# Kernel tuning notes

Hardware: AMD Instinct MI355X
Metric: run time of the kernel (lower is better)

Reference implementation:

```python
import jax, jax.numpy as jnp
import numpy as np

N = 100000      # nodes
E = 800000      # edges
IN1 = 128       # gcn input feature dim
IN2 = 64        # lstm input feature dim
H = 128         # hidden_channels
B = 32          # lstm batch
T = 200         # lstm seq len
OUT = 1         # out_channels
TARGET = jnp.array([0, 1000, 2000, 3000, 4000, 5000, 6000, 7000])  # numgcnE=8


def setup_inputs() -> dict:
    key = jax.random.key(0)
    ks = jax.random.split(key, 20)
    s = 0.05
    inp = {
        "data0": jax.random.normal(ks[0], (B, T, IN2), jnp.float32),
        "data1": jax.random.normal(ks[1], (N, IN1), jnp.float32),
        "edge_index": jax.random.randint(ks[2], (2, E), 0, N, dtype=jnp.int64),
        # GCNConv layers (weight stored [in, out])
        "W1": jax.random.normal(ks[3], (IN1, H), jnp.float32) * s,
        "b1": jnp.zeros((H,), jnp.float32),
        "W2": jax.random.normal(ks[4], (H, H), jnp.float32) * s,
        "b2": jnp.zeros((H,), jnp.float32),
        # LSTM1 (gate order i,f,g,o as in torch)
        "Wih1": jax.random.normal(ks[5], (4 * H, IN2), jnp.float32) * s,
        "Whh1": jax.random.normal(ks[6], (4 * H, H), jnp.float32) * s,
        "bih1": jnp.zeros((4 * H,), jnp.float32),
        "bhh1": jnp.zeros((4 * H,), jnp.float32),
        # LSTM2
        "Wih2": jax.random.normal(ks[7], (4 * H, H), jnp.float32) * s,
        "Whh2": jax.random.normal(ks[8], (4 * H, H), jnp.float32) * s,
        "bih2": jnp.zeros((4 * H,), jnp.float32),
        "bhh2": jnp.zeros((4 * H,), jnp.float32),
        # MLP head: (numgcnE+1)*H -> (numgcnE+1)*H/2 -> OUT
        "m1_w": jax.random.normal(ks[9], (9 * H, 9 * H // 2), jnp.float32) * s,
        "m1_b": jnp.zeros((9 * H // 2,), jnp.float32),
        "m2_w": jax.random.normal(ks[10], (9 * H // 2, OUT), jnp.float32) * s,
        "m2_b": jnp.zeros((OUT,), jnp.float32),
    }
    return inp


def gcn_conv(x, W, b, src, dst, n):
    # PyG GCNConv: self-loops + symmetric normalization, then scatter-add.
    xw = x @ W                                                     # [N, H]
    ones = jnp.ones(src.shape[0], xw.dtype)
    deg = jax.ops.segment_sum(ones, dst, num_segments=n) + 1.0     # +1 self-loop
    dinv = jax.lax.rsqrt(deg)                                      # [N]
    norm = dinv[src] * dinv[dst]                                   # [E]
    agg = jax.ops.segment_sum(xw[src] * norm[:, None], dst, num_segments=n)
    agg = agg + xw * (dinv * dinv)[:, None]                        # self-loop msgs
    return agg + b


def lstm_final(x_tbi, Wih, Whh, bih, bhh):
    # x_tbi: [T, Bsz, in]; returns final hidden state h_T [Bsz, H]
    Bsz = x_tbi.shape[1]
    Hh = Whh.shape[1]
    bias = bih + bhh

    def step(carry, xt):
        h, c = carry
        g = xt @ Wih.T + h @ Whh.T + bias                          # [Bsz, 4H]
        i, f, gg, o = jnp.split(g, 4, axis=-1)
        c = jax.nn.sigmoid(f) * c + jax.nn.sigmoid(i) * jnp.tanh(gg)
        h = jax.nn.sigmoid(o) * jnp.tanh(c)
        return (h, c), None

    init = (jnp.zeros((Bsz, Hh), x_tbi.dtype), jnp.zeros((Bsz, Hh), x_tbi.dtype))
    (h, c), _ = jax.lax.scan(step, init, x_tbi)
    return h


def reference(data0, data1, edge_index, W1, b1, W2, b2,
              Wih1, Whh1, bih1, bhh1, Wih2, Whh2, bih2, bhh2,
              m1_w, m1_b, m2_w, m2_b):
    src, dst = edge_index[0], edge_index[1]
    n = data1.shape[0]
    # two GCN layers with ReLU
    h = jax.nn.relu(gcn_conv(data1, W1, b1, src, dst, n))
    h = jax.nn.relu(gcn_conv(h, W2, b2, src, dst, n))
    g = h[TARGET].reshape(-1)                                      # [numgcnE*H]
    # lstm1 over [B, T, IN2] (batch_first) -> final h_n [B, H]
    h1 = lstm_final(jnp.swapaxes(data0, 0, 1), Wih1, Whh1, bih1, bhh1)
    # lstm2 consumes h_n[None] as [batch=1, seq=B, H] -> final h [1, H]
    h2 = lstm_final(h1[:, None, :], Wih2, Whh2, bih2, bhh2)[0]     # [H]
    d = jnp.concatenate([g, h2])                                   # [(numgcnE+1)*H]
    return (d @ m1_w + m1_b) @ m2_w + m2_b                         # [OUT]
```

## Files before the change

### kernel.cpp

```cpp
#include <hip/hip_runtime.h>
#include <hip/hip_bf16.h>
#include <cstring>

using bf16 = __hip_bfloat16;
typedef _Float16 h2v __attribute__((ext_vector_type(2)));
typedef _Float16 h8v __attribute__((ext_vector_type(8)));

#if __has_builtin(__builtin_amdgcn_fdot2)
__device__ __forceinline__ float FDOT2(h2v a, h2v b, float c) {
    return __builtin_amdgcn_fdot2(a, b, c, false);
}
#else
__device__ __forceinline__ float FDOT2(h2v a, h2v b, float c) {
    return c + (float)a.x * (float)b.x + (float)a.y * (float)b.y;
}
#endif

__device__ __forceinline__ float sigm_f(float x) {
    return __builtin_amdgcn_rcpf(1.f + __expf(-x));
}
__device__ __forceinline__ float tanh_f(float x) {
    return 1.f - 2.f * __builtin_amdgcn_rcpf(1.f + __expf(2.f * x));
}

__device__ __forceinline__ float xor32_get(float x) {
#if __has_builtin(__builtin_amdgcn_permlane32_swap)
    typedef unsigned uv2 __attribute__((ext_vector_type(2)));
    union { float f; unsigned u; } cv; cv.f = x;
    uv2 r = __builtin_amdgcn_permlane32_swap(cv.u, cv.u, false, false);
    union { unsigned u; float f; } rv; rv.u = r[1];
    return rv.f;
#else
    return __shfl_xor(x, 32);
#endif
}

constexpr int NH    = 128;
constexpr int G4    = 512;
constexpr int TSEQ  = 200;
constexpr int BBATCH= 32;
constexpr int NTGT  = 8;

constexpr int LCAP1 = 1024;
constexpr int S1CAP = LCAP1 + NTGT;
constexpr int LCAP2 = 8192;
constexpr int S2CAP = LCAP2 + S1CAP;

constexpr size_t algn(size_t x) { return (x + 255) & ~size_t(255); }
constexpr size_t OFF_GX1  = 0;
constexpr size_t OFF_GX2  = algn(OFF_GX1  + 6400ull * G4 * 4);
constexpr size_t OFF_DEG  = algn(OFF_GX2  + 32ull * G4 * 4);
constexpr size_t OFF_DINV = algn(OFF_DEG  + 100000ull * 4);
constexpr size_t OFF_SL1  = algn(OFF_DINV + 100000ull * 4);
constexpr size_t OFF_SL2  = algn(OFF_SL1  + 100000ull * 4);
constexpr size_t OFF_CNT  = algn(OFF_SL2  + 100000ull * 4);
constexpr size_t OFF_L1   = algn(OFF_CNT  + 64);
constexpr size_t OFF_S1   = algn(OFF_L1   + (size_t)LCAP1 * 8);
constexpr size_t OFF_L2   = algn(OFF_S1   + (size_t)S1CAP * 4);
constexpr size_t OFF_S2   = algn(OFF_L2   + (size_t)LCAP2 * 8);
constexpr size_t OFF_XW1  = algn(OFF_S2   + (size_t)S2CAP * 4);
constexpr size_t OFF_H1   = algn(OFF_XW1  + (size_t)S2CAP * NH * 4);
constexpr size_t OFF_XW2  = algn(OFF_H1   + (size_t)S1CAP * NH * 4);
constexpr size_t OFF_DVEC = algn(OFF_XW2  + (size_t)S1CAP * NH * 4);
constexpr size_t OFF_H1F  = algn(OFF_DVEC + 1152ull * 4);
constexpr size_t OFF_CACC = algn(OFF_H1F  + 32ull * NH * 4);
constexpr size_t WS_NEEDED = OFF_CACC + 576ull * 4;

__device__ __forceinline__ int edge_at(const int* ei, int E, int is64, int row, int e) {
    return is64 ? ei[(((size_t)row * E) + e) * 2] : ei[((size_t)row * E) + e];
}

__device__ __forceinline__ float dinv_of(const int* deg, int v) {
    return rsqrtf((float)deg[v] + 1.0f);
}

__global__ void k_init(const int* ei, int* deg, int* slot1, int* slot2, int* cnt,
                       float* h1, int n, unsigned int* out, unsigned int canary) {
    int i0 = blockIdx.x * 256 + threadIdx.x;
    int gstride = gridDim.x * 256;
    if (i0 < 14) cnt[i0] = 0;
    if (i0 == 15) cnt[15] = (ei[1] == 0 && ei[3] == 0 && ei[5] == 0 && ei[7] == 0) ? 1 : 0;
    if (i0 == 16) out[0] = canary;
    for (int i = i0; i < S1CAP * NH; i += gstride) h1[i] = 0.f;
    for (int i = i0; i < n; i += gstride) { deg[i] = 0; slot1[i] = -1; slot2[i] = -1; }
}

__global__ void k_deg_l1(const int* ei, int E, int* deg, int2* l1, int* cnt) {
    int is64 = cnt[15];
    for (int e = blockIdx.x * 256 + threadIdx.x; e < E; e += gridDim.x * 256) {
        int d = edge_at(ei, E, is64, 1, e);
        if ((unsigned)d < 100000u) atomicAdd(&deg[d], 1);
        if (d <= 7000 && d >= 0 && d % 1000 == 0) {
            int s = edge_at(ei, E, is64, 0, e);
            int idx = atomicAdd(&cnt[0], 1);
            if (idx < LCAP1) l1[idx] = make_int2(s, d);
        }
    }
}

__global__ void k_s1(const int2* l1, int* cnt, int* slot1, int* s1list,
                     int* slot2, int* s2list) {
    __shared__ int ns1;
    if (threadIdx.x == 0) ns1 = 0;
    __syncthreads();
    int m = min(cnt[0], LCAP1);
    for (int i = threadIdx.x; i < NTGT + m; i += blockDim.x) {
        int v = (i < NTGT) ? i * 1000 : l1[i - NTGT].x;
        if ((unsigned)v >= 100000u) continue;
        int old = atomicCAS(&slot1[v], -1, -2);
        if (old == -1) {
            int idx = atomicAdd(&ns1, 1);
            if (idx < S1CAP) { s1list[idx] = v; atomicExch(&slot1[v], idx); }
        }
    }
    __syncthreads();
    int n1 = min(ns1, S1CAP);
    if (threadIdx.x == 0) cnt[1] = n1;
    for (int i = threadIdx.x; i < n1; i += blockDim.x) {
        int v = s1list[i];
        int old = atomicCAS(&slot2[v], -1, -2);
        if (old == -1) {
            int idx = atomicAdd(&cnt[2], 1);
            if (idx < S2CAP) { s2list[idx] = v; atomicExch(&slot2[v], idx); }
        }
    }
}

__global__ void k_l2(const int* ei, int E, const int* slot1,
                     int2* l2, int* cnt, int* slot2, int* s2list) {
    int is64 = cnt[15];
    for (int e = blockIdx.x * 256 + threadIdx.x; e < E; e += gridDim.x * 256) {
        int d = edge_at(ei, E, is64, 1, e);
        if ((unsigned)d >= 100000u) continue;
        if (slot1[d] >= 0) {
            int s = edge_at(ei, E, is64, 0, e);
            if ((unsigned)s >= 100000u) continue;
            int idx = atomicAdd(&cnt[3], 1);
            if (idx < LCAP2) l2[idx] = make_int2(s, d);
            int old = atomicCAS(&slot2[s], -1, -2);
            if (old == -1) {
                int j = atomicAdd(&cnt[2], 1);
                if (j < S2CAP) { s2list[j] = s; atomicExch(&slot2[s], j); }
            }
        }
    }
}


__global__ void k_xw1(const float* x, const float* W, const int* s2list, const int* cnt, float* xw1) {
    int i = blockIdx.x;
    if (i >= min(cnt[2], S2CAP)) return;
    int node = s2list[i];
    __shared__ float xs[NH];
    int c = threadIdx.x;
    xs[c] = x[(size_t)node * NH + c];
    __syncthreads();
    float acc = 0.f;
    #pragma unroll 8
    for (int k = 0; k < NH; k++) acc += xs[k] * W[(size_t)k * NH + c];
    xw1[(size_t)i * NH + c] = acc;
}

__global__ void k_h1scat(const float* xw1, const int2* l2, const int* cnt,
                         const int* slot1, const int* slot2, const int* deg, float* h1) {
    int e = blockIdx.x;
    if (e >= min(cnt[3], LCAP2)) return;
    int2 sd = l2[e];
    int t1 = slot1[sd.y], s2 = slot2[sd.x];
    if (t1 < 0 || t1 >= S1CAP || s2 < 0 || s2 >= S2CAP) return;
    float w = dinv_of(deg, sd.x) * dinv_of(deg, sd.y);
    atomicAdd(&h1[t1 * NH + threadIdx.x],
              xw1[(size_t)s2 * NH + threadIdx.x] * w);
}

__global__ void k_xw2(const float* h1, const float* xw1, const float* W, const float* b1,
                      const int* cnt, const int* s1list, const int* slot2, const int* deg,
                      float* xw2) {
    int i = blockIdx.x;
    if (i >= min(cnt[1], S1CAP)) return;
    __shared__ float xs[NH];
    int c = threadIdx.x;
    int node = s1list[i];
    int s2i = slot2[node];
    if (s2i < 0 || s2i >= S2CAP) s2i = 0;
    float v = dinv_of(deg, node);
    xs[c] = fmaxf(h1[i * NH + c] + xw1[(size_t)s2i * NH + c] * (v * v) + b1[c], 0.f);
    __syncthreads();
    float acc = 0.f;
    #pragma unroll 8
    for (int k = 0; k < NH; k++) acc += xs[k] * W[(size_t)k * NH + c];
    xw2[(size_t)i * NH + c] = acc;
}

__global__ void k_gout(const float* xw2, const int2* l1, const int* cnt,
                       const int* slot1, const int* deg, const float* b2, float* dvec) {
    int t = blockIdx.x;
    int tgt = t * 1000;
    int c = threadIdx.x;
    float vt = dinv_of(deg, tgt);
    int st = slot1[tgt]; if (st < 0 || st >= S1CAP) st = 0;
    float acc = xw2[(size_t)st * NH + c] * vt * vt;
    int m = min(cnt[0], LCAP1);
    for (int e = 0; e < m; e++) {
        int2 sd = l1[e];
        if (sd.y == tgt) {
            int ss = slot1[sd.x];
            if (ss >= 0 && ss < S1CAP)
                acc += xw2[(size_t)ss * NH + c] * dinv_of(deg, sd.x) * vt;
        }
    }
    acc += b2[c];
    dvec[t * NH + c] = fmaxf(acc, 0.f);
}


__global__ __launch_bounds__(256) void k_gx1hw(const float* data0, const float* Wih,
                                               const float* bih, const float* bhh, float* gx,
                                               const float* m1w, const float* m1b,
                                               const float* m2w, const float* m2b, float* hw) {
    int tid = threadIdx.x;
    if (blockIdx.x >= 800) {
        int hb = blockIdx.x - 800;
        int wv = tid >> 6, ln = tid & 63;
        if (hb < 18) {
            #pragma unroll 4
            for (int rr = 0; rr < 16; rr++) {
                int row = hb * 64 + wv * 16 + rr;
                float s = 0.f;
                #pragma unroll
                for (int j = ln; j < 576; j += 64) s += m1w[(size_t)row * 576 + j] * m2w[j];
                #pragma unroll
                for (int off = 32; off > 0; off >>= 1) s += __shfl_down(s, off, 64);
                if (ln == 0) hw[row] = s;
            }
        } else if (wv == 0) {
            float s = 0.f;
            for (int j = ln; j < 576; j += 64) s += m1b[j] * m2w[j];
            #pragma unroll
            for (int off = 32; off > 0; off >>= 1) s += __shfl_down(s, off, 64);
            if (ln == 0) hw[1152] = s + m2b[0];
        }
        return;
    }
    constexpr int LDP = 68;
    __shared__ float As[64 * LDP];
    __shared__ float Bs[64 * LDP];
    int rb = blockIdx.x >> 3;
    int gb = blockIdx.x & 7;
    int r0 = rb * 64, g0 = gb * 64;
    for (int i = tid; i < 64 * 64; i += 256) {
        int rr = i >> 6, k = i & 63;
        int r = r0 + rr, b = r & 31, t = r >> 5;
        As[rr * LDP + k] = data0[((size_t)b * TSEQ + t) * 64 + k];
        Bs[rr * LDP + k] = Wih[(size_t)(g0 + rr) * 64 + k];
    }
    __syncthreads();
    int tr = (tid & 15) * 4;
    int tg = (tid >> 4) * 4;
    float acc[4][4] = {};
    #pragma unroll
    for (int k4 = 0; k4 < 16; k4++) {
        float4 a0 = *(const float4*)&As[(tr + 0) * LDP + k4 * 4];
        float4 a1 = *(const float4*)&As[(tr + 1) * LDP + k4 * 4];
        float4 a2 = *(const float4*)&As[(tr + 2) * LDP + k4 * 4];
        float4 a3 = *(const float4*)&As[(tr + 3) * LDP + k4 * 4];
        float4 b0 = *(const float4*)&Bs[(tg + 0) * LDP + k4 * 4];
        float4 b1 = *(const float4*)&Bs[(tg + 1) * LDP + k4 * 4];
        float4 b2 = *(const float4*)&Bs[(tg + 2) * LDP + k4 * 4];
        float4 b3 = *(const float4*)&Bs[(tg + 3) * LDP + k4 * 4];
        const float4 av[4] = {a0, a1, a2, a3};
        const float4 bv[4] = {b0, b1, b2, b3};
        #pragma unroll
        for (int i = 0; i < 4; i++)
            #pragma unroll
            for (int j = 0; j < 4; j++)
                acc[i][j] += av[i].x * bv[j].x + av[i].y * bv[j].y
                           + av[i].z * bv[j].z + av[i].w * bv[j].w;
    }
    float bias[4];
    #pragma unroll
    for (int j = 0; j < 4; j++) bias[j] = bih[g0 + tg + j] + bhh[g0 + tg + j];
    #pragma unroll
    for (int i = 0; i < 4; i++) {
        size_t row = (size_t)(r0 + tr + i) * G4 + g0 + tg;
        #pragma unroll
        for (int j = 0; j < 4; j++) gx[row + j] = acc[i][j] + bias[j];
    }
}

template<int T, int NB>
__global__ __launch_bounds__(256, 1) void k_lstm1g(const float* gx, const float* Whh,
                                                   const float* Wih2, const float* bih2,
                                                   const float* bhh2, float* gx2) {
    int b = blockIdx.x;
    int tid = threadIdx.x;
    int w = tid >> 6, l = tid & 63;
    int j = w * 32 + (l & 31);
    int role = l >> 5;
    int r0 = role ? (j + NH) : j;
    int r1 = role ? (j + 3 * NH) : (j + 2 * NH);
    __shared__ __align__(16) _Float16 hbuf[2][NH];
    __shared__ float hfin[NH];
    h2v w0[NH / 2], w1[NH / 2];
    #pragma unroll
    for (int k = 0; k < NH; k += 4) {
        float4 a = *(const float4*)&Whh[(size_t)r0 * NH + k];
        w0[k / 2]     = h2v{(_Float16)a.x, (_Float16)a.y};
        w0[k / 2 + 1] = h2v{(_Float16)a.z, (_Float16)a.w};
        float4 c4 = *(const float4*)&Whh[(size_t)r1 * NH + k];
        w1[k / 2]     = h2v{(_Float16)c4.x, (_Float16)c4.y};
        w1[k / 2 + 1] = h2v{(_Float16)c4.z, (_Float16)c4.w};
    }
    if (tid < NH) { hbuf[0][tid] = (_Float16)0.f; hbuf[1][tid] = (_Float16)0.f; }
    float c = 0.f, hout = 0.f;
    float nx0 = gx[((size_t)0 * NB + b) * G4 + r0];
    float nx1 = gx[((size_t)0 * NB + b) * G4 + r1];
    __syncthreads();
    for (int t = 0; t < T; t++) {
        const h8v* hv8 = (const h8v*)hbuf[t & 1];
        float a0 = nx0, a1 = nx1;
        int tn = (t + 1 < T) ? (t + 1) : t;
        nx0 = gx[((size_t)tn * NB + b) * G4 + r0];
        nx1 = gx[((size_t)tn * NB + b) * G4 + r1];
        float p0 = 0.f, q0 = 0.f, p1 = 0.f, q1 = 0.f;
        #pragma unroll
        for (int m = 0; m < NH / 8; m++) {
            h8v h8 = hv8[m];
            h2v ha = __builtin_shufflevector(h8, h8, 0, 1);
            h2v hb = __builtin_shufflevector(h8, h8, 2, 3);
            h2v hc = __builtin_shufflevector(h8, h8, 4, 5);
            h2v hd = __builtin_shufflevector(h8, h8, 6, 7);
            p0 = FDOT2(w0[4 * m],     ha, p0);
            q0 = FDOT2(w0[4 * m + 1], hb, q0);
            p0 = FDOT2(w0[4 * m + 2], hc, p0);
            q0 = FDOT2(w0[4 * m + 3], hd, q0);
            p1 = FDOT2(w1[4 * m],     ha, p1);
            q1 = FDOT2(w1[4 * m + 1], hb, q1);
            p1 = FDOT2(w1[4 * m + 2], hc, p1);
            q1 = FDOT2(w1[4 * m + 3], hd, q1);
        }
        float ga = a0 + p0 + q0;
        float gb = a1 + p1 + q1;
        float s  = sigm_f(ga);
        float tg = role ? sigm_f(gb) : tanh_f(gb);
        float u  = s * tg;
        float fv = xor32_get(s);
        float ov = xor32_get(tg);
        if (role == 0) {
            c = fv * c + u;
            hout = ov * tanh_f(c);
            hbuf[(t + 1) & 1][j] = (_Float16)hout;
        }
        __syncthreads();
    }
    if (role == 0) hfin[j] = hout;
    __syncthreads();
    int g0 = tid, g1 = tid + 256;
    float a0 = bih2[g0] + bhh2[g0];
    float a1 = bih2[g1] + bhh2[g1];
    #pragma unroll 4
    for (int k = 0; k < NH; k++) {
        float hk = hfin[k];
        a0 += Wih2[(size_t)g0 * NH + k] * hk;
        a1 += Wih2[(size_t)g1 * NH + k] * hk;
    }
    gx2[(size_t)b * G4 + g0] = a0;
    gx2[(size_t)b * G4 + g1] = a1;
}

__global__ __launch_bounds__(256, 1) void k_lstm2h(const float* gx, const float* Whh,
                                                   const float* dvec, const float* hw,
                                                   unsigned int* out) {
    constexpr int T = BBATCH;
    int tid = threadIdx.x;
    int w = tid >> 6, l = tid & 63;
    int j = w * 32 + (l & 31);
    int role = l >> 5;
    int r0 = role ? (j + NH) : j;
    int r1 = role ? (j + 3 * NH) : (j + 2 * NH);
    __shared__ __align__(16) _Float16 hbuf[2][NH];
    __shared__ float harr[NH];
    __shared__ float red[4];
    h2v w0[NH / 2], w1[NH / 2];
    #pragma unroll
    for (int k = 0; k < NH; k += 4) {
        float4 a = *(const float4*)&Whh[(size_t)r0 * NH + k];
        w0[k / 2]     = h2v{(_Float16)a.x, (_Float16)a.y};
        w0[k / 2 + 1] = h2v{(_Float16)a.z, (_Float16)a.w};
        float4 c4 = *(const float4*)&Whh[(size_t)r1 * NH + k];
        w1[k / 2]     = h2v{(_Float16)c4.x, (_Float16)c4.y};
        w1[k / 2 + 1] = h2v{(_Float16)c4.z, (_Float16)c4.w};
    }
    if (tid < NH) { hbuf[0][tid] = (_Float16)0.f; hbuf[1][tid] = (_Float16)0.f; }
    float c = 0.f, hout = 0.f;
    float nx0 = gx[r0];
    float nx1 = gx[r1];
    __syncthreads();
    for (int t = 0; t < T; t++) {
        const h8v* hv8 = (const h8v*)hbuf[t & 1];
        float a0 = nx0, a1 = nx1;
        int tn = (t + 1 < T) ? (t + 1) : t;
        nx0 = gx[(size_t)tn * G4 + r0];
        nx1 = gx[(size_t)tn * G4 + r1];
        float p0 = 0.f, q0 = 0.f, p1 = 0.f, q1 = 0.f;
        #pragma unroll
        for (int m = 0; m < NH / 8; m++) {
            h8v h8 = hv8[m];
            h2v ha = __builtin_shufflevector(h8, h8, 0, 1);
            h2v hb = __builtin_shufflevector(h8, h8, 2, 3);
            h2v hc = __builtin_shufflevector(h8, h8, 4, 5);
            h2v hd = __builtin_shufflevector(h8, h8, 6, 7);
            p0 = FDOT2(w0[4 * m],     ha, p0);
            q0 = FDOT2(w0[4 * m + 1], hb, q0);
            p0 = FDOT2(w0[4 * m + 2], hc, p0);
            q0 = FDOT2(w0[4 * m + 3], hd, q0);
            p1 = FDOT2(w1[4 * m],     ha, p1);
            q1 = FDOT2(w1[4 * m + 1], hb, q1);
            p1 = FDOT2(w1[4 * m + 2], hc, p1);
            q1 = FDOT2(w1[4 * m + 3], hd, q1);
        }
        float ga = a0 + p0 + q0;
        float gb = a1 + p1 + q1;
        float s  = sigm_f(ga);
        float tg = role ? sigm_f(gb) : tanh_f(gb);
        float u  = s * tg;
        float fv = xor32_get(s);
        float ov = xor32_get(tg);
        if (role == 0) {
            c = fv * c + u;
            hout = ov * tanh_f(c);
            hbuf[(t + 1) & 1][j] = (_Float16)hout;
        }
        __syncthreads();
    }
    if (role == 0) harr[j] = hout;
    __syncthreads();
    float s = 0.f;
    for (int i = tid; i < 1024; i += 256) s += dvec[i] * hw[i];
    if (tid < NH) s += harr[tid] * hw[1024 + tid];
    #pragma unroll
    for (int off = 32; off > 0; off >>= 1) s += __shfl_down(s, off, 64);
    if ((tid & 63) == 0) red[tid >> 6] = s;
    __syncthreads();
    if (tid == 0) {
        float tot = red[0] + red[1] + red[2] + red[3] + hw[1152];
        bf16 hb = __float2bfloat16(tot);
        unsigned short u;
        memcpy(&u, &hb, 2);
        out[0] = ((unsigned int)u << 16) | u;
    }
}


extern "C" void kernel_launch(void* const* d_in, const int* in_sizes, int n_in,
                              void* d_out, int out_size, void* d_ws, size_t ws_size,
                              hipStream_t stream) {
    const float* data0 = (const float*)d_in[0];
    const float* data1 = (const float*)d_in[1];
    const int*   ei    = (const int*)d_in[2];
    const float* W1    = (const float*)d_in[3];
    const float* b1    = (const float*)d_in[4];
    const float* W2    = (const float*)d_in[5];
    const float* b2    = (const float*)d_in[6];
    const float* Wih1  = (const float*)d_in[7];
    const float* Whh1  = (const float*)d_in[8];
    const float* bih1  = (const float*)d_in[9];
    const float* bhh1  = (const float*)d_in[10];
    const float* Wih2  = (const float*)d_in[11];
    const float* Whh2  = (const float*)d_in[12];
    const float* bih2  = (const float*)d_in[13];
    const float* bhh2  = (const float*)d_in[14];
    const float* m1w   = (const float*)d_in[15];
    const float* m1b   = (const float*)d_in[16];
    const float* m2w   = (const float*)d_in[17];
    const float* m2b   = (const float*)d_in[18];

    const int n = in_sizes[1] / NH;
    const int E = in_sizes[2] / 2;

    char* ws = (char*)d_ws;
    float* gx1   = (float*)(ws + OFF_GX1);
    float* gx2   = (float*)(ws + OFF_GX2);
    int*   deg   = (int*)  (ws + OFF_DEG);
    float* hw    = (float*)(ws + OFF_DINV);
    int*   slot1 = (int*)  (ws + OFF_SL1);
    int*   slot2 = (int*)  (ws + OFF_SL2);
    int*   cnt   = (int*)  (ws + OFF_CNT);
    int2*  l1    = (int2*) (ws + OFF_L1);
    int*   s1l   = (int*)  (ws + OFF_S1);
    int2*  l2    = (int2*) (ws + OFF_L2);
    int*   s2l   = (int*)  (ws + OFF_S2);
    float* xw1   = (float*)(ws + OFF_XW1);
    float* h1    = (float*)(ws + OFF_H1);
    float* xw2   = (float*)(ws + OFF_XW2);
    float* dvec  = (float*)(ws + OFF_DVEC);

    float v = 1.0f + (ws_size < WS_NEEDED ? 1.0f : 0.0f) + (n_in != 19 ? 2.0f : 0.0f);
    unsigned int fb; memcpy(&fb, &v, 4);
    unsigned int hi = fb >> 16;
    unsigned int canary_bits = (hi << 16) | hi;

    int nb = (n + 255) / 256;
    int eb = (E + 255) / 256;

    k_init   <<<nb, 256, 0, stream>>>(ei, deg, slot1, slot2, cnt, h1, n,
                                      (unsigned int*)d_out, canary_bits);
    k_deg_l1 <<<eb, 256, 0, stream>>>(ei, E, deg, l1, cnt);
    k_s1     <<<1, 256, 0, stream>>>(l1, cnt, slot1, s1l, slot2, s2l);
    k_l2     <<<eb, 256, 0, stream>>>(ei, E, slot1, l2, cnt, slot2, s2l);
    k_xw1    <<<S2CAP, NH, 0, stream>>>(data1, W1, s2l, cnt, xw1);
    k_h1scat <<<LCAP2, NH, 0, stream>>>(xw1, l2, cnt, slot1, slot2, deg, h1);
    k_xw2    <<<S1CAP, NH, 0, stream>>>(h1, xw1, W2, b1, cnt, s1l, slot2, deg, xw2);
    k_gout   <<<NTGT, NH, 0, stream>>>(xw2, l1, cnt, slot1, deg, b2, dvec);
    k_gx1hw  <<<819, 256, 0, stream>>>(data0, Wih1, bih1, bhh1, gx1,
                                       m1w, m1b, m2w, m2b, hw);
    k_lstm1g<TSEQ, BBATCH><<<BBATCH, 256, 0, stream>>>(gx1, Whh1, Wih2, bih2, bhh2, gx2);
    k_lstm2h <<<1, 256, 0, stream>>>(gx2, Whh2, dvec, hw, (unsigned int*)d_out);
    (void)out_size;
}
```

Before: 421.8 us.

## Split LSTM recurrence over K halves with permlane reduction instead of gate rows

Each lane pair now computes all four gates for a hidden unit over half of the K dimension, and the two halves are combined with permlane32_swap sums. Before, each lane handled two gate rows over the full K. This halves the LDS h-vector reads per lane per step and shortens the dot-product chains, at the cost of extra cross-lane swaps per step. The xor32_get helper is rewritten to derive the partner value from the swap results, and the Wih2 projection uses float4 loads.

After: 419.1 us. About the same (-0.6%).

```diff
diff --git a/kernel.cpp b/kernel.cpp
--- a/kernel.cpp
+++ b/kernel.cpp
@@ -28,10 +28,22 @@
     typedef unsigned uv2 __attribute__((ext_vector_type(2)));
     union { float f; unsigned u; } cv; cv.f = x;
     uv2 r = __builtin_amdgcn_permlane32_swap(cv.u, cv.u, false, false);
-    union { unsigned u; float f; } rv; rv.u = r[1];
-    return rv.f;
+    union { unsigned u; float f; } ra, rb; ra.u = r[0]; rb.u = r[1];
+    return (ra.f + rb.f) - x;
 #else
     return __shfl_xor(x, 32);
+#endif
+}
+
+__device__ __forceinline__ float half_sum(float x) {
+#if __has_builtin(__builtin_amdgcn_permlane32_swap)
+    typedef unsigned uv2 __attribute__((ext_vector_type(2)));
+    union { float f; unsigned u; } cv; cv.f = x;
+    uv2 r = __builtin_amdgcn_permlane32_swap(cv.u, cv.u, false, false);
+    union { unsigned u; float f; } ra, rb; ra.u = r[0]; rb.u = r[1];
+    return ra.f + rb.f;
+#else
+    return x + __shfl_xor(x, 32);
 #endif
 }
 
@@ -296,73 +308,95 @@
     int tid = threadIdx.x;
     int w = tid >> 6, l = tid & 63;
     int j = w * 32 + (l & 31);
-    int role = l >> 5;
-    int r0 = role ? (j + NH) : j;
-    int r1 = role ? (j + 3 * NH) : (j + 2 * NH);
+    int hf = l >> 5;
+    int k0 = hf * 64;
     __shared__ __align__(16) _Float16 hbuf[2][NH];
     __shared__ float hfin[NH];
-    h2v w0[NH / 2], w1[NH / 2];
+    h2v wi[32], wf[32], wg[32], wo[32];
     #pragma unroll
-    for (int k = 0; k < NH; k += 4) {
-        float4 a = *(const float4*)&Whh[(size_t)r0 * NH + k];
-        w0[k / 2]     = h2v{(_Float16)a.x, (_Float16)a.y};
-        w0[k / 2 + 1] = h2v{(_Float16)a.z, (_Float16)a.w};
-        float4 c4 = *(const float4*)&Whh[(size_t)r1 * NH + k];
-        w1[k / 2]     = h2v{(_Float16)c4.x, (_Float16)c4.y};
-        w1[k / 2 + 1] = h2v{(_Float16)c4.z, (_Float16)c4.w};
+    for (int k = 0; k < 64; k += 4) {
+        float4 a;
+        a = *(const float4*)&Whh[(size_t)j * NH + k0 + k];
+        wi[k / 2] = h2v{(_Float16)a.x, (_Float16)a.y};
+        wi[k / 2 + 1] = h2v{(_Float16)a.z, (_Float16)a.w};
+        a = *(const float4*)&Whh[(size_t)(j + NH) * NH + k0 + k];
+        wf[k / 2] = h2v{(_Float16)a.x, (_Float16)a.y};
+        wf[k / 2 + 1] = h2v{(_Float16)a.z, (_Float16)a.w};
+        a = *(const float4*)&Whh[(size_t)(j + 2 * NH) * NH + k0 + k];
+        wg[k / 2] = h2v{(_Float16)a.x, (_Float16)a.y};
+        wg[k / 2 + 1] = h2v{(_Float16)a.z, (_Float16)a.w};
+        a = *(const float4*)&Whh[(size_t)(j + 3 * NH) * NH + k0 + k];
+        wo[k / 2] = h2v{(_Float16)a.x, (_Float16)a.y};
+        wo[k / 2 + 1] = h2v{(_Float16)a.z, (_Float16)a.w};
     }
     if (tid < NH) { hbuf[0][tid] = (_Float16)0.f; hbuf[1][tid] = (_Float16)0.f; }
     float c = 0.f, hout = 0.f;
-    float nx0 = gx[((size_t)0 * NB + b) * G4 + r0];
-    float nx1 = gx[((size_t)0 * NB + b) * G4 + r1];
+    const float* gp0 = &gx[(size_t)b * G4];
+    float nx0 = gp0[j], nx1 = gp0[j + NH], nx2 = gp0[j + 2 * NH], nx3 = gp0[j + 3 * NH];
     __syncthreads();
     for (int t = 0; t < T; t++) {
-        const h8v* hv8 = (const h8v*)hbuf[t & 1];
-        float a0 = nx0, a1 = nx1;
+        const h8v* hv8 = (const h8v*)&hbuf[t & 1][k0];
+        float a0 = nx0, a1 = nx1, a2 = nx2, a3 = nx3;
         int tn = (t + 1 < T) ? (t + 1) : t;
-        nx0 = gx[((size_t)tn * NB + b) * G4 + r0];
-        nx1 = gx[((size_t)tn * NB + b) * G4 + r1];
-        float p0 = 0.f, q0 = 0.f, p1 = 0.f, q1 = 0.f;
+        const float* gp = &gx[((size_t)tn * NB + b) * G4];
+        nx0 = gp[j]; nx1 = gp[j + NH]; nx2 = gp[j + 2 * NH]; nx3 = gp[j + 3 * NH];
+        float pi = 0.f, qi = 0.f, pf = 0.f, qf = 0.f;
+        float pg = 0.f, qg = 0.f, po = 0.f, qo = 0.f;
         #pragma unroll
-        for (int m = 0; m < NH / 8; m++) {
+        for (int m = 0; m < 8; m++) {
             h8v h8 = hv8[m];
             h2v ha = __builtin_shufflevector(h8, h8, 0, 1);
             h2v hb = __builtin_shufflevector(h8, h8, 2, 3);
             h2v hc = __builtin_shufflevector(h8, h8, 4, 5);
             h2v hd = __builtin_shufflevector(h8, h8, 6, 7);
-            p0 = FDOT2(w0[4 * m],     ha, p0);
-            q0 = FDOT2(w0[4 * m + 1], hb, q0);
-            p0 = FDOT2(w0[4 * m + 2], hc, p0);
-            q0 = FDOT2(w0[4 * m + 3], hd, q0);
-            p1 = FDOT2(w1[4 * m],     ha, p1);
-            q1 = FDOT2(w1[4 * m + 1], hb, q1);
-            p1 = FDOT2(w1[4 * m + 2], hc, p1);
-            q1 = FDOT2(w1[4 * m + 3], hd, q1);
-        }
-        float ga = a0 + p0 + q0;
-        float gb = a1 + p1 + q1;
-        float s  = sigm_f(ga);
-        float tg = role ? sigm_f(gb) : tanh_f(gb);
+            pi = FDOT2(wi[4 * m],     ha, pi);
+            qi = FDOT2(wi[4 * m + 1], hb, qi);
+            pi = FDOT2(wi[4 * m + 2], hc, pi);
+            qi = FDOT2(wi[4 * m + 3], hd, qi);
+            pf = FDOT2(wf[4 * m],     ha, pf);
+            qf = FDOT2(wf[4 * m + 1], hb, qf);
+            pf = FDOT2(wf[4 * m + 2], hc, pf);
+            qf = FDOT2(wf[4 * m + 3], hd, qf);
+            pg = FDOT2(wg[4 * m],     ha, pg);
+            qg = FDOT2(wg[4 * m + 1], hb, qg);
+            pg = FDOT2(wg[4 * m + 2], hc, pg);
+            qg = FDOT2(wg[4 * m + 3], hd, qg);
+            po = FDOT2(wo[4 * m],     ha, po);
+            qo = FDOT2(wo[4 * m + 1], hb, qo);
+            po = FDOT2(wo[4 * m + 2], hc, po);
+            qo = FDOT2(wo[4 * m + 3], hd, qo);
+        }
+        float gi = a0 + half_sum(pi + qi);
+        float gf = a1 + half_sum(pf + qf);
+        float gg = a2 + half_sum(pg + qg);
+        float go = a3 + half_sum(po + qo);
+        float s  = sigm_f(hf ? gf : gi);
+        float tg = hf ? sigm_f(go) : tanh_f(gg);
         float u  = s * tg;
         float fv = xor32_get(s);
         float ov = xor32_get(tg);
-        if (role == 0) {
+        if (hf == 0) {
             c = fv * c + u;
             hout = ov * tanh_f(c);
             hbuf[(t + 1) & 1][j] = (_Float16)hout;
         }
         __syncthreads();
     }
-    if (role == 0) hfin[j] = hout;
+    if (hf == 0) hfin[j] = hout;
     __syncthreads();
     int g0 = tid, g1 = tid + 256;
     float a0 = bih2[g0] + bhh2[g0];
     float a1 = bih2[g1] + bhh2[g1];
-    #pragma unroll 4
-    for (int k = 0; k < NH; k++) {
-        float hk = hfin[k];
-        a0 += Wih2[(size_t)g0 * NH + k] * hk;
-        a1 += Wih2[(size_t)g1 * NH + k] * hk;
+    const float4* w0p = (const float4*)&Wih2[(size_t)g0 * NH];
+    const float4* w1p = (const float4*)&Wih2[(size_t)g1 * NH];
+    const float4* hp  = (const float4*)hfin;
+    #pragma unroll 8
+    for (int k4 = 0; k4 < NH / 4; k4++) {
+        float4 h4 = hp[k4];
+        float4 wa = w0p[k4];
+        float4 wb = w1p[k4];
+        a0 += wa.x * h4.x + wa.y * h4.y + wa.z * h4.z + wa.w * h4.w;
+        a1 += wb.x * h4.x + wb.y * h4.y + wb.z * h4.z + wb.w * h4.w;
     }
     gx2[(size_t)b * G4 + g0] = a0;
     gx2[(size_t)b * G4 + g1] = a1;
@@ -375,65 +409,81 @@
     int tid = threadIdx.x;
     int w = tid >> 6, l = tid & 63;
     int j = w * 32 + (l & 31);
-    int role = l >> 5;
-    int r0 = role ? (j + NH) : j;
-    int r1 = role ? (j + 3 * NH) : (j + 2 * NH);
+    int hf = l >> 5;
+    int k0 = hf * 64;
     __shared__ __align__(16) _Float16 hbuf[2][NH];
     __shared__ float harr[NH];
     __shared__ float red[4];
-    h2v w0[NH / 2], w1[NH / 2];
+    h2v wi[32], wf[32], wg[32], wo[32];
     #pragma unroll
-    for (int k = 0; k < NH; k += 4) {
-        float4 a = *(const float4*)&Whh[(size_t)r0 * NH + k];
-        w0[k / 2]     = h2v{(_Float16)a.x, (_Float16)a.y};
-        w0[k / 2 + 1] = h2v{(_Float16)a.z, (_Float16)a.w};
-        float4 c4 = *(const float4*)&Whh[(size_t)r1 * NH + k];
-        w1[k / 2]     = h2v{(_Float16)c4.x, (_Float16)c4.y};
-        w1[k / 2 + 1] = h2v{(_Float16)c4.z, (_Float16)c4.w};
+    for (int k = 0; k < 64; k += 4) {
+        float4 a;
+        a = *(const float4*)&Whh[(size_t)j * NH + k0 + k];
+        wi[k / 2] = h2v{(_Float16)a.x, (_Float16)a.y};
+        wi[k / 2 + 1] = h2v{(_Float16)a.z, (_Float16)a.w};
+        a = *(const float4*)&Whh[(size_t)(j + NH) * NH + k0 + k];
+        wf[k / 2] = h2v{(_Float16)a.x, (_Float16)a.y};
+        wf[k / 2 + 1] = h2v{(_Float16)a.z, (_Float16)a.w};
+        a = *(const float4*)&Whh[(size_t)(j + 2 * NH) * NH + k0 + k];
+        wg[k / 2] = h2v{(_Float16)a.x, (_Float16)a.y};
+        wg[k / 2 + 1] = h2v{(_Float16)a.z, (_Float16)a.w};
+        a = *(const float4*)&Whh[(size_t)(j + 3 * NH) * NH + k0 + k];
+        wo[k / 2] = h2v{(_Float16)a.x, (_Float16)a.y};
+        wo[k / 2 + 1] = h2v{(_Float16)a.z, (_Float16)a.w};
     }
     if (tid < NH) { hbuf[0][tid] = (_Float16)0.f; hbuf[1][tid] = (_Float16)0.f; }
     float c = 0.f, hout = 0.f;
-    float nx0 = gx[r0];
-    float nx1 = gx[r1];
+    float nx0 = gx[j], nx1 = gx[j + NH], nx2 = gx[j + 2 * NH], nx3 = gx[j + 3 * NH];
     __syncthreads();
     for (int t = 0; t < T; t++) {
-        const h8v* hv8 = (const h8v*)hbuf[t & 1];
-        float a0 = nx0, a1 = nx1;
+        const h8v* hv8 = (const h8v*)&hbuf[t & 1][k0];
+        float a0 = nx0, a1 = nx1, a2 = nx2, a3 = nx3;
         int tn = (t + 1 < T) ? (t + 1) : t;
-        nx0 = gx[(size_t)tn * G4 + r0];
-        nx1 = gx[(size_t)tn * G4 + r1];
-        float p0 = 0.f, q0 = 0.f, p1 = 0.f, q1 = 0.f;
+        const float* gp = &gx[(size_t)tn * G4];
+        nx0 = gp[j]; nx1 = gp[j + NH]; nx2 = gp[j + 2 * NH]; nx3 = gp[j + 3 * NH];
+        float pi = 0.f, qi = 0.f, pf = 0.f, qf = 0.f;
+        float pg = 0.f, qg = 0.f, po = 0.f, qo = 0.f;
         #pragma unroll
-        for (int m = 0; m < NH / 8; m++) {
+        for (int m = 0; m < 8; m++) {
             h8v h8 = hv8[m];
             h2v ha = __builtin_shufflevector(h8, h8, 0, 1);
             h2v hb = __builtin_shufflevector(h8, h8, 2, 3);
             h2v hc = __builtin_shufflevector(h8, h8, 4, 5);
             h2v hd = __builtin_shufflevector(h8, h8, 6, 7);
-            p0 = FDOT2(w0[4 * m],     ha, p0);
-            q0 = FDOT2(w0[4 * m + 1], hb, q0);
-            p0 = FDOT2(w0[4 * m + 2], hc, p0);
-            q0 = FDOT2(w0[4 * m + 3], hd, q0);
-            p1 = FDOT2(w1[4 * m],     ha, p1);
-            q1 = FDOT2(w1[4 * m + 1], hb, q1);
-            p1 = FDOT2(w1[4 * m + 2], hc, p1);
-            q1 = FDOT2(w1[4 * m + 3], hd, q1);
-        }
-        float ga = a0 + p0 + q0;
-        float gb = a1 + p1 + q1;
-        float s  = sigm_f(ga);
-        float tg = role ? sigm_f(gb) : tanh_f(gb);
+            pi = FDOT2(wi[4 * m],     ha, pi);
+            qi = FDOT2(wi[4 * m + 1], hb, qi);
+            pi = FDOT2(wi[4 * m + 2], hc, pi);
+            qi = FDOT2(wi[4 * m + 3], hd, qi);
+            pf = FDOT2(wf[4 * m],     ha, pf);
+            qf = FDOT2(wf[4 * m + 1], hb, qf);
+            pf = FDOT2(wf[4 * m + 2], hc, pf);
+            qf = FDOT2(wf[4 * m + 3], hd, qf);
+            pg = FDOT2(wg[4 * m],     ha, pg);
+            qg = FDOT2(wg[4 * m + 1], hb, qg);
+            pg = FDOT2(wg[4 * m + 2], hc, pg);
+            qg = FDOT2(wg[4 * m + 3], hd, qg);
+            po = FDOT2(wo[4 * m],     ha, po);
+            qo = FDOT2(wo[4 * m + 1], hb, qo);
+            po = FDOT2(wo[4 * m + 2], hc, po);
+            qo = FDOT2(wo[4 * m + 3], hd, qo);
+        }
+        float gi = a0 + half_sum(pi + qi);
+        float gf = a1 + half_sum(pf + qf);
+        float gg = a2 + half_sum(pg + qg);
+        float go = a3 + half_sum(po + qo);
+        float s  = sigm_f(hf ? gf : gi);
+        float tg = hf ? sigm_f(go) : tanh_f(gg);
         float u  = s * tg;
         float fv = xor32_get(s);
         float ov = xor32_get(tg);
-        if (role == 0) {
+        if (hf == 0) {
             c = fv * c + u;
             hout = ov * tanh_f(c);
             hbuf[(t + 1) & 1][j] = (_Float16)hout;
         }
         __syncthreads();
     }
-    if (role == 0) harr[j] = hout;
+    if (hf == 0) harr[j] = hout;
     __syncthreads();
     float s = 0.f;
     for (int i = tid; i < 1024; i += 256) s += dvec[i] * hw[i];
```

## Split LSTM recurrent dot products over K across 512 threads in fp32

Applied to the files above, without the earlier changes.

Both LSTM recurrence kernels now launch 512 threads per block instead of 256. Each gate row's 128-long dot product is split into two 64-element halves held in fp32 registers, and the halves are combined with a lane shuffle. The fp16 fdot2 path and the half-precision hidden buffer are replaced by plain fp32 FMAs and an fp32 shared buffer. The aim is more waves per block for latency hiding, with fewer weight elements per thread on the serial per-step critical path. In exchange the code adds an extra shuffle and a wider block barrier every step, and the permlane swap helper is rewritten to work whichever half a lane sits in.

After: 464.6 us. +10.2%, slower.

```diff
diff --git a/kernel.cpp b/kernel.cpp
--- a/kernel.cpp
+++ b/kernel.cpp
@@ -3,18 +3,6 @@
 #include <cstring>
 
 using bf16 = __hip_bfloat16;
-typedef _Float16 h2v __attribute__((ext_vector_type(2)));
-typedef _Float16 h8v __attribute__((ext_vector_type(8)));
-
-#if __has_builtin(__builtin_amdgcn_fdot2)
-__device__ __forceinline__ float FDOT2(h2v a, h2v b, float c) {
-    return __builtin_amdgcn_fdot2(a, b, c, false);
-}
-#else
-__device__ __forceinline__ float FDOT2(h2v a, h2v b, float c) {
-    return c + (float)a.x * (float)b.x + (float)a.y * (float)b.y;
-}
-#endif
 
 __device__ __forceinline__ float sigm_f(float x) {
     return __builtin_amdgcn_rcpf(1.f + __expf(-x));
@@ -28,8 +16,8 @@
     typedef unsigned uv2 __attribute__((ext_vector_type(2)));
     union { float f; unsigned u; } cv; cv.f = x;
     uv2 r = __builtin_amdgcn_permlane32_swap(cv.u, cv.u, false, false);
-    union { unsigned u; float f; } rv; rv.u = r[1];
-    return rv.f;
+    union { unsigned u; float f; } ra, rb; ra.u = r[0]; rb.u = r[1];
+    return (ra.f + rb.f) - x;
 #else
     return __shfl_xor(x, 32);
 #endif
@@ -289,161 +277,159 @@
 }
 
 template<int T, int NB>
-__global__ __launch_bounds__(256, 1) void k_lstm1g(const float* gx, const float* Whh,
+__global__ __launch_bounds__(512, 2) void k_lstm1n(const float* gx, const float* Whh,
                                                    const float* Wih2, const float* bih2,
                                                    const float* bhh2, float* gx2) {
     int b = blockIdx.x;
     int tid = threadIdx.x;
     int w = tid >> 6, l = tid & 63;
-    int j = w * 32 + (l & 31);
+    int j = w * 16 + (l & 15);
+    int kh = (l >> 4) & 1;
+    int k0 = kh * 64;
     int role = l >> 5;
-    int r0 = role ? (j + NH) : j;
-    int r1 = role ? (j + 3 * NH) : (j + 2 * NH);
-    __shared__ __align__(16) _Float16 hbuf[2][NH];
+    int rowA = role ? (j + NH) : j;
+    int rowB = role ? (j + 3 * NH) : (j + 2 * NH);
+    __shared__ __align__(16) float hbuf[2][NH];
     __shared__ float hfin[NH];
-    h2v w0[NH / 2], w1[NH / 2];
+    float wA[64], wB[64];
     #pragma unroll
-    for (int k = 0; k < NH; k += 4) {
-        float4 a = *(const float4*)&Whh[(size_t)r0 * NH + k];
-        w0[k / 2]     = h2v{(_Float16)a.x, (_Float16)a.y};
-        w0[k / 2 + 1] = h2v{(_Float16)a.z, (_Float16)a.w};
-        float4 c4 = *(const float4*)&Whh[(size_t)r1 * NH + k];
-        w1[k / 2]     = h2v{(_Float16)c4.x, (_Float16)c4.y};
-        w1[k / 2 + 1] = h2v{(_Float16)c4.z, (_Float16)c4.w};
-    }
-    if (tid < NH) { hbuf[0][tid] = (_Float16)0.f; hbuf[1][tid] = (_Float16)0.f; }
+    for (int k = 0; k < 64; k += 4) {
+        float4 a = *(const float4*)&Whh[(size_t)rowA * NH + k0 + k];
+        wA[k] = a.x; wA[k + 1] = a.y; wA[k + 2] = a.z; wA[k + 3] = a.w;
+        float4 c4 = *(const float4*)&Whh[(size_t)rowB * NH + k0 + k];
+        wB[k] = c4.x; wB[k + 1] = c4.y; wB[k + 2] = c4.z; wB[k + 3] = c4.w;
+    }
+    if (tid < NH) { hbuf[0][tid] = 0.f; hbuf[1][tid] = 0.f; }
     float c = 0.f, hout = 0.f;
-    float nx0 = gx[((size_t)0 * NB + b) * G4 + r0];
-    float nx1 = gx[((size_t)0 * NB + b) * G4 + r1];
+    const float* gp0 = &gx[(size_t)b * G4];
+    float nxA = gp0[rowA], nxB = gp0[rowB];
     __syncthreads();
     for (int t = 0; t < T; t++) {
-        const h8v* hv8 = (const h8v*)hbuf[t & 1];
-        float a0 = nx0, a1 = nx1;
+        const float4* hv = (const float4*)&hbuf[t & 1][k0];
+        float aA = nxA, aB = nxB;
         int tn = (t + 1 < T) ? (t + 1) : t;
-        nx0 = gx[((size_t)tn * NB + b) * G4 + r0];
-        nx1 = gx[((size_t)tn * NB + b) * G4 + r1];
-        float p0 = 0.f, q0 = 0.f, p1 = 0.f, q1 = 0.f;
+        const float* gp = &gx[((size_t)tn * NB + b) * G4];
+        nxA = gp[rowA]; nxB = gp[rowB];
+        float pA0 = 0.f, pA1 = 0.f, pB0 = 0.f, pB1 = 0.f;
         #pragma unroll
-        for (int m = 0; m < NH / 8; m++) {
-            h8v h8 = hv8[m];
-            h2v ha = __builtin_shufflevector(h8, h8, 0, 1);
-            h2v hb = __builtin_shufflevector(h8, h8, 2, 3);
-            h2v hc = __builtin_shufflevector(h8, h8, 4, 5);
-            h2v hd = __builtin_shufflevector(h8, h8, 6, 7);
-            p0 = FDOT2(w0[4 * m],     ha, p0);
-            q0 = FDOT2(w0[4 * m + 1], hb, q0);
-            p0 = FDOT2(w0[4 * m + 2], hc, p0);
-            q0 = FDOT2(w0[4 * m + 3], hd, q0);
-            p1 = FDOT2(w1[4 * m],     ha, p1);
-            q1 = FDOT2(w1[4 * m + 1], hb, q1);
-            p1 = FDOT2(w1[4 * m + 2], hc, p1);
-            q1 = FDOT2(w1[4 * m + 3], hd, q1);
-        }
-        float ga = a0 + p0 + q0;
-        float gb = a1 + p1 + q1;
-        float s  = sigm_f(ga);
-        float tg = role ? sigm_f(gb) : tanh_f(gb);
+        for (int m = 0; m < 16; m++) {
+            float4 h4 = hv[m];
+            pA0 = fmaf(wA[4 * m],     h4.x, pA0);
+            pA1 = fmaf(wA[4 * m + 1], h4.y, pA1);
+            pA0 = fmaf(wA[4 * m + 2], h4.z, pA0);
+            pA1 = fmaf(wA[4 * m + 3], h4.w, pA1);
+            pB0 = fmaf(wB[4 * m],     h4.x, pB0);
+            pB1 = fmaf(wB[4 * m + 1], h4.y, pB1);
+            pB0 = fmaf(wB[4 * m + 2], h4.z, pB0);
+            pB1 = fmaf(wB[4 * m + 3], h4.w, pB1);
+        }
+        float pA = pA0 + pA1, pB = pB0 + pB1;
+        pA += __shfl_xor(pA, 16, 64);
+        pB += __shfl_xor(pB, 16, 64);
+        float gA = aA + pA;
+        float gB = aB + pB;
+        float s  = sigm_f(gA);
+        float tg = role ? sigm_f(gB) : tanh_f(gB);
         float u  = s * tg;
         float fv = xor32_get(s);
         float ov = xor32_get(tg);
         if (role == 0) {
             c = fv * c + u;
             hout = ov * tanh_f(c);
-            hbuf[(t + 1) & 1][j] = (_Float16)hout;
+            if (kh == 0) hbuf[(t + 1) & 1][j] = hout;
         }
         __syncthreads();
     }
-    if (role == 0) hfin[j] = hout;
-    __syncthreads();
-    int g0 = tid, g1 = tid + 256;
-    float a0 = bih2[g0] + bhh2[g0];
-    float a1 = bih2[g1] + bhh2[g1];
-    #pragma unroll 4
-    for (int k = 0; k < NH; k++) {
-        float hk = hfin[k];
-        a0 += Wih2[(size_t)g0 * NH + k] * hk;
-        a1 += Wih2[(size_t)g1 * NH + k] * hk;
-    }
-    gx2[(size_t)b * G4 + g0] = a0;
-    gx2[(size_t)b * G4 + g1] = a1;
-}
-
-__global__ __launch_bounds__(256, 1) void k_lstm2h(const float* gx, const float* Whh,
+    if (l < 16) hfin[j] = hout;
+    __syncthreads();
+    int g = tid;
+    float a0 = bih2[g] + bhh2[g];
+    const float4* wp = (const float4*)&Wih2[(size_t)g * NH];
+    const float4* hp = (const float4*)hfin;
+    #pragma unroll 8
+    for (int k4 = 0; k4 < NH / 4; k4++) {
+        float4 h4 = hp[k4];
+        float4 wv = wp[k4];
+        a0 += wv.x * h4.x + wv.y * h4.y + wv.z * h4.z + wv.w * h4.w;
+    }
+    gx2[(size_t)b * G4 + g] = a0;
+}
+
+__global__ __launch_bounds__(512, 2) void k_lstm2n(const float* gx, const float* Whh,
                                                    const float* dvec, const float* hw,
                                                    unsigned int* out) {
     constexpr int T = BBATCH;
     int tid = threadIdx.x;
     int w = tid >> 6, l = tid & 63;
-    int j = w * 32 + (l & 31);
+    int j = w * 16 + (l & 15);
+    int kh = (l >> 4) & 1;
+    int k0 = kh * 64;
     int role = l >> 5;
-    int r0 = role ? (j + NH) : j;
-    int r1 = role ? (j + 3 * NH) : (j + 2 * NH);
-    __shared__ __align__(16) _Float16 hbuf[2][NH];
+    int rowA = role ? (j + NH) : j;
+    int rowB = role ? (j + 3 * NH) : (j + 2 * NH);
+    __shared__ __align__(16) float hbuf[2][NH];
     __shared__ float harr[NH];
-    __shared__ float red[4];
-    h2v w0[NH / 2], w1[NH / 2];
+    __shared__ float red[8];
+    float wA[64], wB[64];
     #pragma unroll
-    for (int k = 0; k < NH; k += 4) {
-        float4 a = *(const float4*)&Whh[(size_t)r0 * NH + k];
-        w0[k / 2]     = h2v{(_Float16)a.x, (_Float16)a.y};
-        w0[k / 2 + 1] = h2v{(_Float16)a.z, (_Float16)a.w};
-        float4 c4 = *(const float4*)&Whh[(size_t)r1 * NH + k];
-        w1[k / 2]     = h2v{(_Float16)c4.x, (_Float16)c4.y};
-        w1[k / 2 + 1] = h2v{(_Float16)c4.z, (_Float16)c4.w};
-    }
-    if (tid < NH) { hbuf[0][tid] = (_Float16)0.f; hbuf[1][tid] = (_Float16)0.f; }
+    for (int k = 0; k < 64; k += 4) {
+        float4 a = *(const float4*)&Whh[(size_t)rowA * NH + k0 + k];
+        wA[k] = a.x; wA[k + 1] = a.y; wA[k + 2] = a.z; wA[k + 3] = a.w;
+        float4 c4 = *(const float4*)&Whh[(size_t)rowB * NH + k0 + k];
+        wB[k] = c4.x; wB[k + 1] = c4.y; wB[k + 2] = c4.z; wB[k + 3] = c4.w;
+    }
+    if (tid < NH) { hbuf[0][tid] = 0.f; hbuf[1][tid] = 0.f; }
     float c = 0.f, hout = 0.f;
-    float nx0 = gx[r0];
-    float nx1 = gx[r1];
+    float nxA = gx[rowA], nxB = gx[rowB];
     __syncthreads();
     for (int t = 0; t < T; t++) {
-        const h8v* hv8 = (const h8v*)hbuf[t & 1];
-        float a0 = nx0, a1 = nx1;
+        const float4* hv = (const float4*)&hbuf[t & 1][k0];
+        float aA = nxA, aB = nxB;
         int tn = (t + 1 < T) ? (t + 1) : t;
-        nx0 = gx[(size_t)tn * G4 + r0];
-        nx1 = gx[(size_t)tn * G4 + r1];
-        float p0 = 0.f, q0 = 0.f, p1 = 0.f, q1 = 0.f;
+        const float* gp = &gx[(size_t)tn * G4];
+        nxA = gp[rowA]; nxB = gp[rowB];
+        float pA0 = 0.f, pA1 = 0.f, pB0 = 0.f, pB1 = 0.f;
         #pragma unroll
-        for (int m = 0; m < NH / 8; m++) {
-            h8v h8 = hv8[m];
-            h2v ha = __builtin_shufflevector(h8, h8, 0, 1);
-            h2v hb = __builtin_shufflevector(h8, h8, 2, 3);
-            h2v hc = __builtin_shufflevector(h8, h8, 4, 5);
-            h2v hd = __builtin_shufflevector(h8, h8, 6, 7);
-            p0 = FDOT2(w0[4 * m],     ha, p0);
-            q0 = FDOT2(w0[4 * m + 1], hb, q0);
-            p0 = FDOT2(w0[4 * m + 2], hc, p0);
-            q0 = FDOT2(w0[4 * m + 3], hd, q0);
-            p1 = FDOT2(w1[4 * m],     ha, p1);
-            q1 = FDOT2(w1[4 * m + 1], hb, q1);
-            p1 = FDOT2(w1[4 * m + 2], hc, p1);
-            q1 = FDOT2(w1[4 * m + 3], hd, q1);
-        }
-        float ga = a0 + p0 + q0;
-        float gb = a1 + p1 + q1;
-        float s  = sigm_f(ga);
-        float tg = role ? sigm_f(gb) : tanh_f(gb);
+        for (int m = 0; m < 16; m++) {
+            float4 h4 = hv[m];
+            pA0 = fmaf(wA[4 * m],     h4.x, pA0);
+            pA1 = fmaf(wA[4 * m + 1], h4.y, pA1);
+            pA0 = fmaf(wA[4 * m + 2], h4.z, pA0);
+            pA1 = fmaf(wA[4 * m + 3], h4.w, pA1);
+            pB0 = fmaf(wB[4 * m],     h4.x, pB0);
+            pB1 = fmaf(wB[4 * m + 1], h4.y, pB1);
+            pB0 = fmaf(wB[4 * m + 2], h4.z, pB0);
+            pB1 = fmaf(wB[4 * m + 3], h4.w, pB1);
+        }
+        float pA = pA0 + pA1, pB = pB0 + pB1;
+        pA += __shfl_xor(pA, 16, 64);
+        pB += __shfl_xor(pB, 16, 64);
+        float gA = aA + pA;
+        float gB = aB + pB;
+        float s  = sigm_f(gA);
+        float tg = role ? sigm_f(gB) : tanh_f(gB);
         float u  = s * tg;
         float fv = xor32_get(s);
         float ov = xor32_get(tg);
         if (role == 0) {
             c = fv * c + u;
             hout = ov * tanh_f(c);
-            hbuf[(t + 1) & 1][j] = (_Float16)hout;
+            if (kh == 0) hbuf[(t + 1) & 1][j] = hout;
         }
         __syncthreads();
     }
-    if (role == 0) harr[j] = hout;
+    if (l < 16) harr[j] = hout;
     __syncthreads();
     float s = 0.f;
-    for (int i = tid; i < 1024; i += 256) s += dvec[i] * hw[i];
+    for (int i = tid; i < 1024; i += 512) s += dvec[i] * hw[i];
     if (tid < NH) s += harr[tid] * hw[1024 + tid];
     #pragma unroll
     for (int off = 32; off > 0; off >>= 1) s += __shfl_down(s, off, 64);
     if ((tid & 63) == 0) red[tid >> 6] = s;
     __syncthreads();
     if (tid == 0) {
-        float tot = red[0] + red[1] + red[2] + red[3] + hw[1152];
+        float tot = red[0] + red[1] + red[2] + red[3]
+                  + red[4] + red[5] + red[6] + red[7] + hw[1152];
         bf16 hb = __float2bfloat16(tot);
         unsigned short u;
         memcpy(&u, &hb, 2);
@@ -514,7 +500,7 @@
     k_gout   <<<NTGT, NH, 0, stream>>>(xw2, l1, cnt, slot1, deg, b2, dvec);
     k_gx1hw  <<<819, 256, 0, stream>>>(data0, Wih1, bih1, bhh1, gx1,
                                        m1w, m1b, m2w, m2b, hw);
-    k_lstm1g<TSEQ, BBATCH><<<BBATCH, 256, 0, stream>>>(gx1, Whh1, Wih2, bih2, bhh2, gx2);
-    k_lstm2h <<<1, 256, 0, stream>>>(gx2, Whh2, dvec, hw, (unsigned int*)d_out);
+    k_lstm1n<TSEQ, BBATCH><<<BBATCH, 512, 0, stream>>>(gx1, Whh1, Wih2, bih2, bhh2, gx2);
+    k_lstm2n <<<1, 512, 0, stream>>>(gx2, Whh2, dvec, hw, (unsigned int*)d_out);
     (void)out_size;
 }
```
